# Optimization experiments

Measured on AMD Instinct MI355X. Metric: run time of the kernel, lower is better.

The kernel has to match this reference:

```python
import jax, jax.numpy as jnp
import numpy as np

B, NQ, NP = 4, 8192, 2048
DIM_INP, DIM, HID, OUT, NBLK = 256, 200, 128, 3, 5
VAR = 0.2 ** 2


def setup_inputs() -> dict:
    key = jax.random.key(0)
    ks = jax.random.split(key, 12)
    s = 0.05  # weight scale to keep activations sane
    return {
        "xyz_q": jax.random.uniform(ks[0], (B, NQ, 3), jnp.float32),
        "anchors": jax.random.uniform(ks[1], (B, NP, 3), jnp.float32),
        "anchor_feats": jax.random.normal(ks[2], (B, NP, DIM_INP), jnp.float32),
        "fc0_w": jax.random.normal(ks[3], (DIM_INP, DIM), jnp.float32) * s,
        "fc0_b": jnp.zeros((DIM,), jnp.float32),
        "fc1_w": jax.random.normal(ks[4], (DIM, HID), jnp.float32) * s,
        "fc1_b": jnp.zeros((HID,), jnp.float32),
        "blk_w0": jax.random.normal(ks[5], (NBLK, HID, HID), jnp.float32) * s,
        "blk_b0": jnp.zeros((NBLK, HID), jnp.float32),
        "blk_w1": jax.random.normal(ks[6], (NBLK, HID, HID), jnp.float32) * s,
        "blk_b1": jnp.zeros((NBLK, HID), jnp.float32),
        "fcc_w": jax.random.normal(ks[7], (NBLK, DIM, HID), jnp.float32) * s,
        "fcc_b": jnp.zeros((NBLK, HID), jnp.float32),
        "out_w": jax.random.normal(ks[8], (HID, OUT), jnp.float32) * s,
        "out_b": jnp.zeros((OUT,), jnp.float32),
    }


def reference(xyz_q, anchors, anchor_feats, fc0_w, fc0_b, fc1_w, fc1_b,
              blk_w0, blk_b0, blk_w1, blk_b1, fcc_w, fcc_b, out_w, out_b):
    relu = jax.nn.relu
    # Gaussian-kernel interpolation of anchor features at query points.
    # diff: [B, nq, np, 3]
    diff = anchors[:, None, :, :] - xyz_q[:, :, None, :]
    d = jnp.linalg.norm(diff, axis=-1)                    # [B, nq, np]
    logits = -((d + 1e-5) ** 2) / VAR
    weight = jax.nn.softmax(logits, axis=2)               # exp / sum, stable
    c = jnp.einsum('bqp,bpd->bqd', weight, anchor_feats)  # [B, nq, dim_inp]
    lat = c @ fc0_w + fc0_b                               # [B, nq, dim]
    net = relu(lat) @ fc1_w + fc1_b                       # [B, nq, hid]
    for i in range(NBLK):
        net = net + lat @ fcc_w[i] + fcc_b[i]
        # ResnetBlockFC: x + fc_1(relu(fc_0(relu(x))))
        dx = relu(relu(net) @ blk_w0[i] + blk_b0[i]) @ blk_w1[i] + blk_b1[i]
        net = net + dx
    return relu(net) @ out_w + out_b                      # [B, nq, 3]
```

## Files before the change

### kernel.cpp

```cpp
#include <hip/hip_runtime.h>
#include <math.h>

#define NP     2048
#define NQTOT  8192
#define DIN    256
#define DIM    200
#define HID    128
#define NOUT3  3
#define NBLK   5
#define TQ     32
#define NTHR   256
#define INVVAR 25.0f
#define NKT    (NP / 32)
#define NDT    (DIN / 16)
#define WSCALE 32768.0f
#define NFRAG  760

using f16x8 = __attribute__((ext_vector_type(8))) _Float16;
using f32x4 = __attribute__((ext_vector_type(4))) float;

__device__ __forceinline__ unsigned int pkrtz_u32(float a, float b) {
  auto p = __builtin_amdgcn_cvt_pkrtz(a, b);
  return __builtin_bit_cast(unsigned int, p);
}
__device__ __forceinline__ void pack_f16_2(const float* f, f16x8& h, f16x8& l) {
#pragma unroll
  for (int j = 0; j < 8; ++j) {
    const float v = f[j];
    const _Float16 hh = (_Float16)v;
    h[j] = hh; l[j] = (_Float16)(v - (float)hh);
  }
}
__device__ __forceinline__ void pack_w16(const float* f, f16x8& h, f16x8& l) {
#pragma unroll
  for (int j = 0; j < 8; ++j) {
    const float v = f[j] * WSCALE;
    const _Float16 hh = (_Float16)v;
    h[j] = hh; l[j] = (_Float16)(v - (float)hh);
  }
}
__device__ __forceinline__ void pack_a(const float* f, f16x8& h, f16x8& l) {
  union { f16x8 v; unsigned int u[4]; } H, L;
#pragma unroll
  for (int jp = 0; jp < 4; ++jp) {
    const float a = f[2 * jp], b = f[2 * jp + 1];
    auto hp = __builtin_amdgcn_cvt_pkrtz(a, b);
    H.u[jp] = __builtin_bit_cast(unsigned int, hp);
    L.u[jp] = pkrtz_u32(a - (float)hp[0], b - (float)hp[1]);
  }
  h = H.v; l = L.v;
}
__device__ __forceinline__ unsigned int split_pack(float x) {
  auto hp = __builtin_amdgcn_cvt_pkrtz(x, x);
  return pkrtz_u32(x, x - (float)hp[0]);
}

__device__ __forceinline__ int qsw(int r, int q) {
  return r * TQ + (q ^ (((r >> 2) & 7) << 2));
}
template<int KPAD>
__device__ __forceinline__ int sidx(int q, int k) {
  return q * KPAD + (((k >> 2) ^ (q & 7)) << 2) + (k & 3);
}

template<int KPAD, bool RELU>
__device__ __forceinline__ void store_split4(unsigned int* dst, int k, int qbase, f32x4 v) {
#pragma unroll
  for (int r = 0; r < 4; ++r) {
    float x = v[r];
    if (RELU) x = fmaxf(x, 0.f);
    dst[sidx<KPAD>(qbase + r, k)] = split_pack(x);
  }
}

__global__ __launch_bounds__(NTHR) void pid_packf(const float* __restrict__ F,
                                                  f16x8* __restrict__ wsHi,
                                                  f16x8* __restrict__ wsLo) {
  const int wid = threadIdx.x >> 6, l = threadIdx.x & 63;
  const int tile = blockIdx.x * 4 + wid;
  const int b  = tile >> 10;
  const int kt = (tile >> 4) & 63;
  const int dt = tile & 15;
  const int grp = l >> 4, qn = l & 15;
  const float* src = F + ((size_t)b * NP + kt * 32 + grp * 8) * DIN + dt * 16 + qn;
  float v[8];
#pragma unroll
  for (int j = 0; j < 8; ++j) v[j] = src[(size_t)j * DIN];
  f16x8 h, lo;
  pack_f16_2(v, h, lo);
  const size_t fi = (size_t)tile * 64 + l;
  wsHi[fi] = h; wsLo[fi] = lo;
}

__global__ __launch_bounds__(NTHR) void pid_packw(
    const float* __restrict__ fc0_w, const float* __restrict__ fc1_w,
    const float* __restrict__ fcc_w, const float* __restrict__ blk_w0,
    const float* __restrict__ blk_w1,
    f16x8* __restrict__ Wh, f16x8* __restrict__ Wm) {
  const int wid = threadIdx.x >> 6, l = threadIdx.x & 63;
  const int f = blockIdx.x * 4 + wid;
  if (f >= NFRAG) return;
  const float* src; int Kl, Nl, ks, nt;
  if (f < 104)      { int r = f;       src = fc0_w; Kl = 256; Nl = 200; ks = r / 13; nt = r % 13; }
  else if (f < 160) { int r = f - 104; src = fc1_w; Kl = 200; Nl = 128; ks = r / 8;  nt = r % 8; }
  else if (f < 440) { int r = f - 160; int i = r / 56; r %= 56;
                      src = fcc_w + (size_t)i * DIM * HID; Kl = 200; Nl = 128; ks = r / 8; nt = r % 8; }
  else if (f < 600) { int r = f - 440; int i = r / 32; r %= 32;
                      src = blk_w0 + (size_t)i * HID * HID; Kl = 128; Nl = 128; ks = r / 8; nt = r % 8; }
  else              { int r = f - 600; int i = r / 32; r %= 32;
                      src = blk_w1 + (size_t)i * HID * HID; Kl = 128; Nl = 128; ks = r / 8; nt = r % 8; }
  const int grp = l >> 4, n = nt * 16 + (l & 15);
  f16x8 h, m;
#pragma unroll
  for (int j = 0; j < 8; ++j) {
    const int k = ks * 32 + grp * 8 + j;
    const float v = (k < Kl && n < Nl) ? src[(size_t)k * Nl + n] : 0.f;
    const _Float16 hh = (_Float16)v;
    h[j] = hh; m[j] = (_Float16)(v - (float)hh);
  }
  const size_t fi = (size_t)f * 64 + l;
  Wh[fi] = h; Wm[fi] = m;
}

template<int KS, int NT, int MAXNT, int KPADIN, bool RELUA>
__device__ __forceinline__ void mm_stage(
    const unsigned int* __restrict__ Xs,
    const f16x8* __restrict__ Wh, const f16x8* __restrict__ Wm, int fbase,
    f32x4 acc[2][MAXNT], int wid, int l) {
  const int grp = l >> 4, qn = l & 15;
#pragma unroll 1
  for (int ks = 0; ks < KS; ++ks) {
    f16x8 bh[MAXNT], bm[MAXNT];
#pragma unroll
    for (int i = 0; i < MAXNT; ++i) {
      const int nt = wid + i * 4;
      if (nt < NT) {
        const size_t fi = (size_t)(fbase + ks * NT + nt) * 64 + l;
        bh[i] = Wh[fi]; bm[i] = Wm[fi];
      }
    }
    const int u0 = ks * 8 + grp * 2;
    f16x8 ah[2], al[2];
#pragma unroll
    for (int qt = 0; qt < 2; ++qt) {
      const int q = qt * 16 + qn;
      const unsigned int* row = Xs + q * KPADIN;
      const uint4 lo = *(const uint4*)(row + (((u0) ^ (q & 7)) << 2));
      const uint4 hi = *(const uint4*)(row + (((u0 + 1) ^ (q & 7)) << 2));
      unsigned int p[8] = {lo.x, lo.y, lo.z, lo.w, hi.x, hi.y, hi.z, hi.w};
      if (RELUA) {
#pragma unroll
        for (int j = 0; j < 8; ++j) p[j] = (p[j] & 0x8000u) ? 0u : p[j];
      }
      union { f16x8 v; unsigned int u[4]; } H, L;
#pragma unroll
      for (int jp = 0; jp < 4; ++jp) {
        H.u[jp] = __builtin_amdgcn_perm(p[2 * jp + 1], p[2 * jp], 0x05040100u);
        L.u[jp] = __builtin_amdgcn_perm(p[2 * jp + 1], p[2 * jp], 0x07060302u);
      }
      ah[qt] = H.v; al[qt] = L.v;
    }
#pragma unroll
    for (int qt = 0; qt < 2; ++qt)
#pragma unroll
      for (int i = 0; i < MAXNT; ++i)
        if (wid + i * 4 < NT) {
          acc[qt][i] = __builtin_amdgcn_mfma_f32_16x16x32_f16(ah[qt], bh[i], acc[qt][i], 0, 0, 0);
          acc[qt][i] = __builtin_amdgcn_mfma_f32_16x16x32_f16(ah[qt], bm[i], acc[qt][i], 0, 0, 0);
          acc[qt][i] = __builtin_amdgcn_mfma_f32_16x16x32_f16(al[qt], bh[i], acc[qt][i], 0, 0, 0);
        }
  }
}

struct SMemV2 {
  union {
    struct { float ax[NP * 3]; float qx[TQ], qy[TQ], qz[TQ]; } a;
    unsigned int lats[32 * 224];
  } r1;
  union {
    unsigned int cTs[32 * 256];
    struct { unsigned int nets[32 * 128]; unsigned int tmps[32 * 128]; } nt;
    float netf[128 * 32];
  } r2;
  float sS[64];
};

__global__ __launch_bounds__(NTHR, 2) void pid_fused_mfma(
    const float* __restrict__ xyz_q, const float* __restrict__ anchors,
    const f16x8* __restrict__ wsFh, const f16x8* __restrict__ wsFl,
    const f16x8* __restrict__ Wh, const f16x8* __restrict__ Wm,
    const float* __restrict__ fc0_b, const float* __restrict__ fc1_b,
    const float* __restrict__ blk_b0, const float* __restrict__ blk_b1,
    const float* __restrict__ fcc_b,
    const float* __restrict__ out_w, const float* __restrict__ out_b,
    float* __restrict__ out) {
  __shared__ SMemV2 sm;
  const int t = threadIdx.x;
  const int bi = blockIdx.x;
  const int batch = bi & 3;
  const int q0 = (bi >> 2) * TQ;

  {
    const float4* src = (const float4*)(anchors + (size_t)batch * NP * 3);
    float4* dst = (float4*)sm.r1.a.ax;
#pragma unroll
    for (int j = 0; j < (NP * 3 / 4) / NTHR; ++j)
      dst[j * NTHR + t] = src[j * NTHR + t];
  }
  if (t < TQ) {
    const float* qp = xyz_q + ((size_t)batch * NQTOT + q0 + t) * 3;
    sm.r1.a.qx[t] = qp[0]; sm.r1.a.qy[t] = qp[1]; sm.r1.a.qz[t] = qp[2];
  }
  __syncthreads();

  const int wid = t >> 6, l = t & 63;
  const int kp = wid & 1;
  const int dh = wid >> 1;
  const int grp = l >> 4, qn = l & 15;
  const float q0x = sm.r1.a.qx[qn],      q0y = sm.r1.a.qy[qn],      q0z = sm.r1.a.qz[qn];
  const float q1x = sm.r1.a.qx[16 + qn], q1y = sm.r1.a.qy[16 + qn], q1z = sm.r1.a.qz[16 + qn];
  const float nC1 = -36.067376f;
  const float nC2 = -7.2134752e-4f;

  const size_t fb = (size_t)batch * (NKT * NDT * 64) + kp * 1024 + dh * 512 + l;
  const f16x8* pH0 = wsFh + fb;  const f16x8* pL0 = wsFl + fb;
  const f16x8* pH1 = pH0 + 256;  const f16x8* pL1 = pL0 + 256;

  f32x4 acc[2][8];
#pragma unroll
  for (int a = 0; a < 2; ++a)
#pragma unroll
    for (int j = 0; j < 8; ++j) acc[a][j] = (f32x4){0.f, 0.f, 0.f, 0.f};
  float s0 = 0.f, s1 = 0.f;

#pragma unroll 1
  for (int kt = kp; kt < NKT; kt += 2) {
    const int pb = kt * 32 + grp * 8;
    float4 av[6];
    {
      const float4* ap = (const float4*)&sm.r1.a.ax[pb * 3];
#pragma unroll
      for (int j = 0; j < 6; ++j) av[j] = ap[j];
    }
    const float* af = (const float*)av;
    float w8[8];
#pragma unroll
    for (int j = 0; j < 8; ++j) {
      const float dx = af[3 * j] - q0x, dy = af[3 * j + 1] - q0y, dz = af[3 * j + 2] - q0z;
      const float D = fmaf(dx, dx, fmaf(dy, dy, dz * dz));
      const float s = __builtin_amdgcn_sqrtf(D);
      const float u = __builtin_amdgcn_exp2f(fmaf(nC2, s, fmaf(nC1, D, 15.0f)));
      w8[j] = u; s0 += u;
    }
    f16x8 ah0, al0;
    pack_a(w8, ah0, al0);
#pragma unroll
    for (int j = 0; j < 8; ++j) {
      const float dx = af[3 * j] - q1x, dy = af[3 * j + 1] - q1y, dz = af[3 * j + 2] - q1z;
      const float D = fmaf(dx, dx, fmaf(dy, dy, dz * dz));
      const float s = __builtin_amdgcn_sqrtf(D);
      const float u = __builtin_amdgcn_exp2f(fmaf(nC2, s, fmaf(nC1, D, 15.0f)));
      w8[j] = u; s1 += u;
    }
    f16x8 ah1, al1;
    pack_a(w8, ah1, al1);

#define CHUNK2(PH, PL, DOFF)                                                  \
    {                                                                         \
      f16x8 bh[4], bl[4];                                                     \
      _Pragma("unroll") for (int k = 0; k < 4; ++k) {                         \
        bh[k] = PH[k * 64]; bl[k] = PL[k * 64];                               \
      }                                                                       \
      _Pragma("unroll") for (int k = 0; k < 4; ++k) {                         \
        f32x4 a0 = acc[0][DOFF + k];                                          \
        a0 = __builtin_amdgcn_mfma_f32_16x16x32_f16(ah0, bh[k], a0, 0, 0, 0); \
        a0 = __builtin_amdgcn_mfma_f32_16x16x32_f16(ah0, bl[k], a0, 0, 0, 0); \
        a0 = __builtin_amdgcn_mfma_f32_16x16x32_f16(al0, bh[k], a0, 0, 0, 0); \
        acc[0][DOFF + k] = a0;                                                \
        f32x4 a1 = acc[1][DOFF + k];                                          \
        a1 = __builtin_amdgcn_mfma_f32_16x16x32_f16(ah1, bh[k], a1, 0, 0, 0); \
        a1 = __builtin_amdgcn_mfma_f32_16x16x32_f16(ah1, bl[k], a1, 0, 0, 0); \
        a1 = __builtin_amdgcn_mfma_f32_16x16x32_f16(al1, bh[k], a1, 0, 0, 0); \
        acc[1][DOFF + k] = a1;                                                \
      }                                                                       \
    }
    CHUNK2(pH0, pL0, 0)
    CHUNK2(pH1, pL1, 4)
#undef CHUNK2
    pH0 += 2048; pL0 += 2048; pH1 += 2048; pL1 += 2048;
  }

  s0 += __shfl_xor(s0, 16); s0 += __shfl_xor(s0, 32);
  s1 += __shfl_xor(s1, 16); s1 += __shfl_xor(s1, 32);
  if (dh == 0 && l < 16) {
    sm.sS[kp * 32 + qn] = s0;
    sm.sS[kp * 32 + 16 + qn] = s1;
  }
  float4* P = (float4*)sm.r2.cTs;
  if (kp == 0) {
#pragma unroll
    for (int qt2 = 0; qt2 < 2; ++qt2)
#pragma unroll
      for (int d2 = 0; d2 < 8; ++d2)
        P[(qt2 * 16 + dh * 8 + d2) * 64 + grp * 16 + qn] =
            make_float4(acc[qt2][d2][0], acc[qt2][d2][1],
                        acc[qt2][d2][2], acc[qt2][d2][3]);
  }
  __syncthreads();
  if (kp == 1) {
#pragma unroll
    for (int qt2 = 0; qt2 < 2; ++qt2)
#pragma unroll
      for (int d2 = 0; d2 < 8; ++d2) {
        const float4 pv = P[(qt2 * 16 + dh * 8 + d2) * 64 + grp * 16 + qn];
        acc[qt2][d2][0] += pv.x; acc[qt2][d2][1] += pv.y;
        acc[qt2][d2][2] += pv.z; acc[qt2][d2][3] += pv.w;
      }
  } else {
    const int lid = (wid >> 1) * 64 + l;
#pragma unroll
    for (int z = 0; z < 6; ++z) {
      const int idx = lid * 6 + z;
      const int q = idx / 24, kk = 200 + idx % 24;
      sm.r1.lats[sidx<224>(q, kk)] = 0u;
    }
  }
  __syncthreads();
  if (kp == 1) {
    float sc0[4], sc1[4];
#pragma unroll
    for (int r = 0; r < 4; ++r) {
      const int j = grp * 4 + r;
      sc0[r] = __builtin_amdgcn_rcpf(sm.sS[j] + sm.sS[32 + j]);
      sc1[r] = __builtin_amdgcn_rcpf(sm.sS[16 + j] + sm.sS[48 + j]);
    }
#pragma unroll
    for (int d2 = 0; d2 < 8; ++d2) {
      const int k = (dh * 8 + d2) * 16 + qn;
      const f32x4 v0 = {acc[0][d2][0] * sc0[0], acc[0][d2][1] * sc0[1],
                        acc[0][d2][2] * sc0[2], acc[0][d2][3] * sc0[3]};
      store_split4<256, false>(sm.r2.cTs, k, grp * 4, v0);
      const f32x4 v1 = {acc[1][d2][0] * sc1[0], acc[1][d2][1] * sc1[1],
                        acc[1][d2][2] * sc1[2], acc[1][d2][3] * sc1[3]};
      store_split4<256, false>(sm.r2.cTs, k, 16 + grp * 4, v1);
    }
  }
  __syncthreads();

  {
    f32x4 a0[2][4];
#pragma unroll
    for (int i = 0; i < 4; ++i) {
      const int nt = wid + i * 4;
      if (nt < 13) {
        const int n = nt * 16 + qn;
        const float b = (n < 200) ? fc0_b[n] : 0.f;
#pragma unroll
        for (int q2 = 0; q2 < 2; ++q2) a0[q2][i] = (f32x4){b, b, b, b};
      }
    }
    mm_stage<8, 13, 4, 256, false>(sm.r2.cTs, Wh, Wm, 0, a0, wid, l);
#pragma unroll
    for (int q2 = 0; q2 < 2; ++q2)
#pragma unroll
      for (int i = 0; i < 4; ++i) {
        const int nt = wid + i * 4;
        if (nt < 13)
          store_split4<224, false>(sm.r1.lats, nt * 16 + qn, q2 * 16 + grp * 4, a0[q2][i]);
      }
  }
  __syncthreads();

  f32x4 net[2][2];
#pragma unroll
  for (int i = 0; i < 2; ++i) {
    const float b = fc1_b[(wid + i * 4) * 16 + qn];
#pragma unroll
    for (int q2 = 0; q2 < 2; ++q2) net[q2][i] = (f32x4){b, b, b, b};
  }
  mm_stage<7, 8, 2, 224, true>(sm.r1.lats, Wh, Wm, 104, net, wid, l);

#pragma unroll 1
  for (int ib = 0; ib < NBLK; ++ib) {
#pragma unroll
    for (int i = 0; i < 2; ++i) {
      const float b = fcc_b[ib * HID + (wid + i * 4) * 16 + qn];
#pragma unroll
      for (int q2 = 0; q2 < 2; ++q2) net[q2][i] += (f32x4){b, b, b, b};
    }
    mm_stage<7, 8, 2, 224, false>(sm.r1.lats, Wh, Wm, 160 + 56 * ib, net, wid, l);
#pragma unroll
    for (int q2 = 0; q2 < 2; ++q2)
#pragma unroll
      for (int i = 0; i < 2; ++i)
        store_split4<128, true>(sm.r2.nt.nets, (wid + i * 4) * 16 + qn,
                                q2 * 16 + grp * 4, net[q2][i]);
    __syncthreads();
    f32x4 a2[2][2];
#pragma unroll
    for (int i = 0; i < 2; ++i) {
      const float b = blk_b0[ib * HID + (wid + i * 4) * 16 + qn];
#pragma unroll
      for (int q2 = 0; q2 < 2; ++q2) a2[q2][i] = (f32x4){b, b, b, b};
    }
    mm_stage<4, 8, 2, 128, false>(sm.r2.nt.nets, Wh, Wm, 440 + 32 * ib, a2, wid, l);
#pragma unroll
    for (int q2 = 0; q2 < 2; ++q2)
#pragma unroll
      for (int i = 0; i < 2; ++i)
        store_split4<128, true>(sm.r2.nt.tmps, (wid + i * 4) * 16 + qn,
                                q2 * 16 + grp * 4, a2[q2][i]);
    __syncthreads();
#pragma unroll
    for (int i = 0; i < 2; ++i) {
      const float b = blk_b1[ib * HID + (wid + i * 4) * 16 + qn];
#pragma unroll
      for (int q2 = 0; q2 < 2; ++q2) net[q2][i] += (f32x4){b, b, b, b};
    }
    mm_stage<4, 8, 2, 128, false>(sm.r2.nt.tmps, Wh, Wm, 600 + 32 * ib, net, wid, l);
    __syncthreads();
  }

#pragma unroll
  for (int q2 = 0; q2 < 2; ++q2)
#pragma unroll
    for (int i = 0; i < 2; ++i) {
      const int n = (wid + i * 4) * 16 + qn;
      *(float4*)&sm.r2.netf[n * 32 + q2 * 16 + grp * 4] =
          make_float4(net[q2][i][0], net[q2][i][1], net[q2][i][2], net[q2][i][3]);
    }
  __syncthreads();
  if (t < TQ * NOUT3) {
    const int q = t / NOUT3, n = t - q * NOUT3;
    float s = out_b[n];
#pragma unroll 8
    for (int k = 0; k < HID; ++k)
      s = fmaf(fmaxf(sm.r2.netf[k * 32 + q], 0.f), out_w[k * NOUT3 + n], s);
    out[((size_t)batch * NQTOT + q0 + q) * NOUT3 + n] = s;
  }
}

template<int K, bool RELUX, bool ACCY>
__device__ __forceinline__ void stage_h128(const float* __restrict__ X,
                                           const float* __restrict__ Wg,
                                           const float* __restrict__ bg,
                                           float* __restrict__ Y, int t) {
  const int qg = t & 7, ng = t >> 3;
  const int n0 = ng * 4, q0 = qg * 4;
  const float4 bv = *(const float4*)&bg[n0];
  const float br[4] = {bv.x, bv.y, bv.z, bv.w};
  float acc[4][4];
#pragma unroll
  for (int j = 0; j < 4; ++j) {
    if (ACCY) {
      const float4 yv = *(const float4*)&Y[qsw(n0 + j, q0)];
      acc[0][j] = yv.x + br[j]; acc[1][j] = yv.y + br[j];
      acc[2][j] = yv.z + br[j]; acc[3][j] = yv.w + br[j];
    } else {
      acc[0][j] = br[j]; acc[1][j] = br[j]; acc[2][j] = br[j]; acc[3][j] = br[j];
    }
  }
#pragma unroll 2
  for (int k0 = 0; k0 < K; k0 += 8) {
    float4 wr[8];
#pragma unroll
    for (int kk = 0; kk < 8; ++kk)
      wr[kk] = *(const float4*)&Wg[(size_t)(k0 + kk) * HID + n0];
#pragma unroll
    for (int kk = 0; kk < 8; ++kk) {
      float4 xv = *(const float4*)&X[qsw(k0 + kk, q0)];
      if (RELUX) {
        xv.x = fmaxf(xv.x, 0.f); xv.y = fmaxf(xv.y, 0.f);
        xv.z = fmaxf(xv.z, 0.f); xv.w = fmaxf(xv.w, 0.f);
      }
      const float xr[4] = {xv.x, xv.y, xv.z, xv.w};
      const float wl[4] = {wr[kk].x, wr[kk].y, wr[kk].z, wr[kk].w};
#pragma unroll
      for (int i = 0; i < 4; ++i)
#pragma unroll
        for (int j = 0; j < 4; ++j)
          acc[i][j] = fmaf(xr[i], wl[j], acc[i][j]);
    }
  }
#pragma unroll
  for (int j = 0; j < 4; ++j)
    *(float4*)&Y[qsw(n0 + j, q0)] =
        make_float4(acc[0][j], acc[1][j], acc[2][j], acc[3][j]);
}

__device__ __forceinline__ void stage_fc0v(const float* __restrict__ X,
                                           const float* __restrict__ Wg,
                                           const float* __restrict__ bg,
                                           float* __restrict__ Y, int t) {
  const int qg = t & 7, ng = t >> 3;
  const int n0 = ng * 8, q0 = qg * 4;
  const bool act = (ng < 25);
  float acc[4][8];
  if (act) {
    const float4 b0 = *(const float4*)&bg[n0];
    const float4 b1 = *(const float4*)&bg[n0 + 4];
    const float br[8] = {b0.x, b0.y, b0.z, b0.w, b1.x, b1.y, b1.z, b1.w};
#pragma unroll
    for (int j = 0; j < 8; ++j)
#pragma unroll
      for (int i = 0; i < 4; ++i) acc[i][j] = br[j];
  }
#pragma unroll 2
  for (int k0 = 0; k0 < DIN; k0 += 4) {
    if (act) {
      float4 wa[4], wb[4];
#pragma unroll
      for (int kk = 0; kk < 4; ++kk) {
        wa[kk] = *(const float4*)&Wg[(size_t)(k0 + kk) * DIM + n0];
        wb[kk] = *(const float4*)&Wg[(size_t)(k0 + kk) * DIM + n0 + 4];
      }
#pragma unroll
      for (int kk = 0; kk < 4; ++kk) {
        const float4 xv = *(const float4*)&X[qsw(k0 + kk, q0)];
        const float xr[4] = {xv.x, xv.y, xv.z, xv.w};
        const float wl[8] = {wa[kk].x, wa[kk].y, wa[kk].z, wa[kk].w,
                             wb[kk].x, wb[kk].y, wb[kk].z, wb[kk].w};
#pragma unroll
        for (int i = 0; i < 4; ++i)
#pragma unroll
          for (int j = 0; j < 8; ++j)
            acc[i][j] = fmaf(xr[i], wl[j], acc[i][j]);
      }
    }
  }
  if (act) {
#pragma unroll
    for (int j = 0; j < 8; ++j)
      *(float4*)&Y[qsw(n0 + j, q0)] =
          make_float4(acc[0][j], acc[1][j], acc[2][j], acc[3][j]);
  }
}

struct SA1 {
  float ax[NP * 3];
  float qx[TQ], qy[TQ], qz[TQ], m[TQ];
  float sred[8 * TQ];
};
struct SB1 {
  float lat[DIM * TQ];
  union {
    float cT[DIN * TQ];
    struct { float net[HID * TQ]; float tmp[HID * TQ]; } nt;
  } u;
};
struct SMem1 { union { SA1 a; SB1 b; } s; float sS[TQ]; };

__global__ __launch_bounds__(NTHR, 2) void pid_fused_vec(
    const float* __restrict__ xyz_q, const float* __restrict__ anchors,
    const f16x8* __restrict__ wsFh, const f16x8* __restrict__ wsFl,
    const float* __restrict__ fc0_w, const float* __restrict__ fc0_b,
    const float* __restrict__ fc1_w, const float* __restrict__ fc1_b,
    const float* __restrict__ blk_w0, const float* __restrict__ blk_b0,
    const float* __restrict__ blk_w1, const float* __restrict__ blk_b1,
    const float* __restrict__ fcc_w, const float* __restrict__ fcc_b,
    const float* __restrict__ out_w, const float* __restrict__ out_b,
    float* __restrict__ out) {
  __shared__ SMem1 sm;
  const int t = threadIdx.x;
  const int bi = blockIdx.x;
  const int batch = bi & 3;
  const int q0 = (bi >> 2) * TQ;

  {
    const float4* src = (const float4*)(anchors + (size_t)batch * NP * 3);
    float4* dst = (float4*)sm.s.a.ax;
#pragma unroll
    for (int j = 0; j < (NP * 3 / 4) / NTHR; ++j)
      dst[j * NTHR + t] = src[j * NTHR + t];
  }
  if (t < TQ) {
    const float* qp = xyz_q + ((size_t)batch * NQTOT + q0 + t) * 3;
    sm.s.a.qx[t] = qp[0]; sm.s.a.qy[t] = qp[1]; sm.s.a.qz[t] = qp[2];
  }
  __syncthreads();
  {
    const int q = t & 31, g = t >> 5;
    const float qxv = sm.s.a.qx[q], qyv = sm.s.a.qy[q], qzv = sm.s.a.qz[q];
    float mloc = 3.0e38f;
    const float* az = sm.s.a.ax + g * 256 * 3;
    for (int pi = 0; pi < 256; ++pi) {
      const float dx = az[pi * 3 + 0] - qxv;
      const float dy = az[pi * 3 + 1] - qyv;
      const float dz = az[pi * 3 + 2] - qzv;
      mloc = fminf(mloc, fmaf(dx, dx, fmaf(dy, dy, dz * dz)));
    }
    sm.s.a.sred[g * TQ + q] = mloc;
  }
  __syncthreads();
  if (t < TQ) {
    float mv = sm.s.a.sred[t];
#pragma unroll
    for (int g = 1; g < 8; ++g) mv = fminf(mv, sm.s.a.sred[g * TQ + t]);
    const float dmin = sqrtf(mv) + 1e-5f;
    sm.s.a.m[t] = -dmin * dmin * INVVAR;
  }
  __syncthreads();

  const int wid = t >> 6, l = t & 63;
  const int qt = wid & 1;
  const int dgb = (wid >> 1) * 8;
  const int grp = l >> 4, qn = l & 15;
  const float qxv = sm.s.a.qx[qt * 16 + qn];
  const float qyv = sm.s.a.qy[qt * 16 + qn];
  const float qzv = sm.s.a.qz[qt * 16 + qn];
  const float negm = -sm.s.a.m[qt * 16 + qn];
  const f16x8* BH = wsFh + (size_t)batch * NKT * NDT * 64;
  const f16x8* BL = wsFl + (size_t)batch * NKT * NDT * 64;

  f32x4 acc[8];
#pragma unroll
  for (int j = 0; j < 8; ++j) acc[j] = (f32x4){0.f, 0.f, 0.f, 0.f};
  float ssum = 0.f;
#pragma unroll 1
  for (int kt = 0; kt < NKT; ++kt) {
    f16x8 bh[8], bl[8];
#pragma unroll
    for (int d2 = 0; d2 < 8; ++d2) {
      const size_t fi = ((size_t)kt * NDT + dgb + d2) * 64 + l;
      bh[d2] = BH[fi]; bl[d2] = BL[fi];
    }
    const int pb = kt * 32 + grp * 8;
    float4 av[6];
    {
      const float4* ap = (const float4*)&sm.s.a.ax[pb * 3];
#pragma unroll
      for (int j = 0; j < 6; ++j) av[j] = ap[j];
    }
    const float* af = (const float*)av;
    float w8[8];
#pragma unroll
    for (int j = 0; j < 8; ++j) {
      const float dx = af[3 * j] - qxv, dy = af[3 * j + 1] - qyv, dz = af[3 * j + 2] - qzv;
      const float d = sqrtf(fmaf(dx, dx, fmaf(dy, dy, dz * dz))) + 1e-5f;
      const float u = __expf(fmaf(d * d, -INVVAR, negm));
      w8[j] = u; ssum += u;
    }
    f16x8 ah, al;
    pack_w16(w8, ah, al);
#pragma unroll
    for (int d2 = 0; d2 < 8; ++d2)
      acc[d2] = __builtin_amdgcn_mfma_f32_16x16x32_f16(ah, bh[d2], acc[d2], 0, 0, 0);
#pragma unroll
    for (int d2 = 0; d2 < 8; ++d2)
      acc[d2] = __builtin_amdgcn_mfma_f32_16x16x32_f16(ah, bl[d2], acc[d2], 0, 0, 0);
#pragma unroll
    for (int d2 = 0; d2 < 8; ++d2)
      acc[d2] = __builtin_amdgcn_mfma_f32_16x16x32_f16(al, bh[d2], acc[d2], 0, 0, 0);
  }
  ssum += __shfl_xor(ssum, 16);
  ssum += __shfl_xor(ssum, 32);
  if (wid < 2 && grp == 0) sm.sS[qt * 16 + qn] = ssum;
  __syncthreads();
  float sc[4];
#pragma unroll
  for (int r = 0; r < 4; ++r)
    sc[r] = (1.0f / WSCALE) / sm.sS[qt * 16 + grp * 4 + r];
#pragma unroll
  for (int d2 = 0; d2 < 8; ++d2) {
    const int d = (dgb + d2) * 16 + qn;
    *(float4*)&sm.s.b.u.cT[qsw(d, qt * 16 + grp * 4)] =
        make_float4(acc[d2][0] * sc[0], acc[d2][1] * sc[1],
                    acc[d2][2] * sc[2], acc[d2][3] * sc[3]);
  }
  __syncthreads();

  stage_fc0v(sm.s.b.u.cT, fc0_w, fc0_b, sm.s.b.lat, t);
  __syncthreads();
  stage_h128<DIM, true, false>(sm.s.b.lat, fc1_w, fc1_b, sm.s.b.u.nt.net, t);
  __syncthreads();
#pragma unroll 1
  for (int i = 0; i < NBLK; ++i) {
    stage_h128<DIM, false, true>(sm.s.b.lat, fcc_w + (size_t)i * DIM * HID,
                                 fcc_b + i * HID, sm.s.b.u.nt.net, t);
    __syncthreads();
    stage_h128<HID, true, false>(sm.s.b.u.nt.net, blk_w0 + (size_t)i * HID * HID,
                                 blk_b0 + i * HID, sm.s.b.u.nt.tmp, t);
    __syncthreads();
    stage_h128<HID, true, true>(sm.s.b.u.nt.tmp, blk_w1 + (size_t)i * HID * HID,
                                blk_b1 + i * HID, sm.s.b.u.nt.net, t);
    __syncthreads();
  }
  if (t < TQ * NOUT3) {
    const int q = t / NOUT3, n = t - q * NOUT3;
    float s = out_b[n];
    const float* net = sm.s.b.u.nt.net;
#pragma unroll 8
    for (int k = 0; k < HID; ++k)
      s = fmaf(fmaxf(net[k * TQ + (q ^ (((k >> 2) & 7) << 2))], 0.f),
               out_w[k * NOUT3 + n], s);
    out[((size_t)batch * NQTOT + q0 + q) * NOUT3 + n] = s;
  }
}

extern "C" void kernel_launch(void* const* d_in, const int* in_sizes, int n_in,
                              void* d_out, int out_size, void* d_ws, size_t ws_size,
                              hipStream_t stream) {
  (void)in_sizes; (void)n_in; (void)out_size;
  const float* xyz_q        = (const float*)d_in[0];
  const float* anchors      = (const float*)d_in[1];
  const float* anchor_feats = (const float*)d_in[2];
  const float* fc0_w        = (const float*)d_in[3];
  const float* fc0_b        = (const float*)d_in[4];
  const float* fc1_w        = (const float*)d_in[5];
  const float* fc1_b        = (const float*)d_in[6];
  const float* blk_w0       = (const float*)d_in[7];
  const float* blk_b0       = (const float*)d_in[8];
  const float* blk_w1       = (const float*)d_in[9];
  const float* blk_b1       = (const float*)d_in[10];
  const float* fcc_w        = (const float*)d_in[11];
  const float* fcc_b        = (const float*)d_in[12];
  const float* out_w        = (const float*)d_in[13];
  const float* out_b        = (const float*)d_in[14];
  float* out = (float*)d_out;

  const size_t F_BYTES = (size_t)4 * NKT * NDT * 64 * 16;
  const size_t W_BYTES = (size_t)NFRAG * 64 * 16;
  f16x8* wsFh = (f16x8*)d_ws;
  f16x8* wsFl = (f16x8*)((char*)d_ws + F_BYTES);
  f16x8* Wh   = (f16x8*)((char*)d_ws + 2 * F_BYTES);
  f16x8* Wm   = (f16x8*)((char*)d_ws + 2 * F_BYTES + W_BYTES);

  hipLaunchKernelGGL(pid_packf, dim3(1024), dim3(NTHR), 0, stream,
                     anchor_feats, wsFh, wsFl);
  if (ws_size >= 2 * F_BYTES + 2 * W_BYTES) {
    hipLaunchKernelGGL(pid_packw, dim3((NFRAG + 3) / 4), dim3(NTHR), 0, stream,
                       fc0_w, fc1_w, fcc_w, blk_w0, blk_w1, Wh, Wm);
    hipLaunchKernelGGL(pid_fused_mfma, dim3(1024), dim3(NTHR), 0, stream,
                       xyz_q, anchors, wsFh, wsFl, Wh, Wm,
                       fc0_b, fc1_b, blk_b0, blk_b1, fcc_b, out_w, out_b, out);
  } else {
    hipLaunchKernelGGL(pid_fused_vec, dim3(1024), dim3(NTHR), 0, stream,
                       xyz_q, anchors, wsFh, wsFl,
                       fc0_w, fc0_b, fc1_w, fc1_b, blk_w0, blk_b0,
                       blk_w1, blk_b1, fcc_w, fcc_b, out_w, out_b, out);
  }
}
```

Before: 262.4 us.

## Prefetch MFMA weight fragments ahead of compute and drop per-block barrier

The MLP stage helper now double-buffers its weight fragments, loading the next k-step's fragments from global memory while MFMAs run on the current ones. The interpolation loop issues all eight weight-fragment loads at the top of each iteration, before the distance and exp work, so global latency hides behind ALU work. The trailing __syncthreads inside the residual-block loop moves after the loop. Each change targets exposed memory latency or barrier stalls, at the cost of more live VGPRs (spill or occupancy risk under launch_bounds 2) and a possible shared-memory race between consecutive blocks if that barrier was needed.

```diff
diff --git a/kernel.cpp b/kernel.cpp
--- a/kernel.cpp
+++ b/kernel.cpp
@@ -128,48 +128,58 @@
     const f16x8* __restrict__ Wh, const f16x8* __restrict__ Wm, int fbase,
     f32x4 acc[2][MAXNT], int wid, int l) {
   const int grp = l >> 4, qn = l & 15;
+  f16x8 bhA[MAXNT], bmA[MAXNT], bhB[MAXNT], bmB[MAXNT];
+
+#define LOADF(BH, BM, KSV)                                                    \
+  _Pragma("unroll") for (int i = 0; i < MAXNT; ++i) {                         \
+    const int nt = wid + i * 4;                                               \
+    if (nt < NT) {                                                            \
+      const size_t fi = (size_t)(fbase + (KSV) * NT + nt) * 64 + l;           \
+      BH[i] = Wh[fi]; BM[i] = Wm[fi];                                         \
+    }                                                                         \
+  }
+
+#define COMPUTE(KSV, BH, BM)                                                  \
+  {                                                                           \
+    const int u0 = (KSV) * 8 + grp * 2;                                       \
+    f16x8 ah[2], al[2];                                                       \
+    _Pragma("unroll") for (int qt = 0; qt < 2; ++qt) {                        \
+      const int q = qt * 16 + qn;                                             \
+      const unsigned int* row = Xs + q * KPADIN;                              \
+      const uint4 lo = *(const uint4*)(row + (((u0) ^ (q & 7)) << 2));        \
+      const uint4 hi = *(const uint4*)(row + (((u0 + 1) ^ (q & 7)) << 2));    \
+      unsigned int p[8] = {lo.x, lo.y, lo.z, lo.w, hi.x, hi.y, hi.z, hi.w};   \
+      if (RELUA) {                                                            \
+        _Pragma("unroll") for (int j = 0; j < 8; ++j)                         \
+          p[j] = (p[j] & 0x8000u) ? 0u : p[j];                                \
+      }                                                                       \
+      union { f16x8 v; unsigned int u[4]; } H, L;                             \
+      _Pragma("unroll") for (int jp = 0; jp < 4; ++jp) {                      \
+        H.u[jp] = __builtin_amdgcn_perm(p[2 * jp + 1], p[2 * jp], 0x05040100u);\
+        L.u[jp] = __builtin_amdgcn_perm(p[2 * jp + 1], p[2 * jp], 0x07060302u);\
+      }                                                                       \
+      ah[qt] = H.v; al[qt] = L.v;                                             \
+    }                                                                         \
+    _Pragma("unroll") for (int qt = 0; qt < 2; ++qt)                          \
+    _Pragma("unroll") for (int i = 0; i < MAXNT; ++i)                         \
+      if (wid + i * 4 < NT) {                                                 \
+        acc[qt][i] = __builtin_amdgcn_mfma_f32_16x16x32_f16(ah[qt], BH[i], acc[qt][i], 0, 0, 0); \
+        acc[qt][i] = __builtin_amdgcn_mfma_f32_16x16x32_f16(ah[qt], BM[i], acc[qt][i], 0, 0, 0); \
+        acc[qt][i] = __builtin_amdgcn_mfma_f32_16x16x32_f16(al[qt], BH[i], acc[qt][i], 0, 0, 0); \
+      }                                                                       \
+  }
+
+  LOADF(bhA, bmA, 0)
 #pragma unroll 1
-  for (int ks = 0; ks < KS; ++ks) {
-    f16x8 bh[MAXNT], bm[MAXNT];
-#pragma unroll
-    for (int i = 0; i < MAXNT; ++i) {
-      const int nt = wid + i * 4;
-      if (nt < NT) {
-        const size_t fi = (size_t)(fbase + ks * NT + nt) * 64 + l;
-        bh[i] = Wh[fi]; bm[i] = Wm[fi];
-      }
-    }
-    const int u0 = ks * 8 + grp * 2;
-    f16x8 ah[2], al[2];
-#pragma unroll
-    for (int qt = 0; qt < 2; ++qt) {
-      const int q = qt * 16 + qn;
-      const unsigned int* row = Xs + q * KPADIN;
-      const uint4 lo = *(const uint4*)(row + (((u0) ^ (q & 7)) << 2));
-      const uint4 hi = *(const uint4*)(row + (((u0 + 1) ^ (q & 7)) << 2));
-      unsigned int p[8] = {lo.x, lo.y, lo.z, lo.w, hi.x, hi.y, hi.z, hi.w};
-      if (RELUA) {
-#pragma unroll
-        for (int j = 0; j < 8; ++j) p[j] = (p[j] & 0x8000u) ? 0u : p[j];
-      }
-      union { f16x8 v; unsigned int u[4]; } H, L;
-#pragma unroll
-      for (int jp = 0; jp < 4; ++jp) {
-        H.u[jp] = __builtin_amdgcn_perm(p[2 * jp + 1], p[2 * jp], 0x05040100u);
-        L.u[jp] = __builtin_amdgcn_perm(p[2 * jp + 1], p[2 * jp], 0x07060302u);
-      }
-      ah[qt] = H.v; al[qt] = L.v;
-    }
-#pragma unroll
-    for (int qt = 0; qt < 2; ++qt)
-#pragma unroll
-      for (int i = 0; i < MAXNT; ++i)
-        if (wid + i * 4 < NT) {
-          acc[qt][i] = __builtin_amdgcn_mfma_f32_16x16x32_f16(ah[qt], bh[i], acc[qt][i], 0, 0, 0);
-          acc[qt][i] = __builtin_amdgcn_mfma_f32_16x16x32_f16(ah[qt], bm[i], acc[qt][i], 0, 0, 0);
-          acc[qt][i] = __builtin_amdgcn_mfma_f32_16x16x32_f16(al[qt], bh[i], acc[qt][i], 0, 0, 0);
-        }
-  }
+  for (int ks = 0; ks + 1 < KS; ks += 2) {
+    LOADF(bhB, bmB, ks + 1)
+    COMPUTE(ks, bhA, bmA)
+    if (ks + 2 < KS) { LOADF(bhA, bmA, ks + 2) }
+    COMPUTE(ks + 1, bhB, bmB)
+  }
+  if (KS & 1) { COMPUTE(KS - 1, bhA, bmA) }
+#undef LOADF
+#undef COMPUTE
 }
 
 struct SMemV2 {
@@ -235,6 +245,12 @@
 
 #pragma unroll 1
   for (int kt = kp; kt < NKT; kt += 2) {
+    f16x8 bh0[4], bl0[4], bh1[4], bl1[4];
+#pragma unroll
+    for (int k = 0; k < 4; ++k) { bh0[k] = pH0[k * 64]; bl0[k] = pL0[k * 64]; }
+#pragma unroll
+    for (int k = 0; k < 4; ++k) { bh1[k] = pH1[k * 64]; bl1[k] = pL1[k * 64]; }
+
     const int pb = kt * 32 + grp * 8;
     float4 av[6];
     {
@@ -265,28 +281,21 @@
     f16x8 ah1, al1;
     pack_a(w8, ah1, al1);
 
-#define CHUNK2(PH, PL, DOFF)                                                  \
-    {                                                                         \
-      f16x8 bh[4], bl[4];                                                     \
-      _Pragma("unroll") for (int k = 0; k < 4; ++k) {                         \
-        bh[k] = PH[k * 64]; bl[k] = PL[k * 64];                               \
-      }                                                                       \
-      _Pragma("unroll") for (int k = 0; k < 4; ++k) {                         \
-        f32x4 a0 = acc[0][DOFF + k];                                          \
-        a0 = __builtin_amdgcn_mfma_f32_16x16x32_f16(ah0, bh[k], a0, 0, 0, 0); \
-        a0 = __builtin_amdgcn_mfma_f32_16x16x32_f16(ah0, bl[k], a0, 0, 0, 0); \
-        a0 = __builtin_amdgcn_mfma_f32_16x16x32_f16(al0, bh[k], a0, 0, 0, 0); \
-        acc[0][DOFF + k] = a0;                                                \
-        f32x4 a1 = acc[1][DOFF + k];                                          \
-        a1 = __builtin_amdgcn_mfma_f32_16x16x32_f16(ah1, bh[k], a1, 0, 0, 0); \
-        a1 = __builtin_amdgcn_mfma_f32_16x16x32_f16(ah1, bl[k], a1, 0, 0, 0); \
-        a1 = __builtin_amdgcn_mfma_f32_16x16x32_f16(al1, bh[k], a1, 0, 0, 0); \
-        acc[1][DOFF + k] = a1;                                                \
-      }                                                                       \
-    }
-    CHUNK2(pH0, pL0, 0)
-    CHUNK2(pH1, pL1, 4)
-#undef CHUNK2
+#define MM3(ACC, AH, AL, BH, BL)                                              \
+    ACC = __builtin_amdgcn_mfma_f32_16x16x32_f16(AH, BH, ACC, 0, 0, 0);       \
+    ACC = __builtin_amdgcn_mfma_f32_16x16x32_f16(AH, BL, ACC, 0, 0, 0);       \
+    ACC = __builtin_amdgcn_mfma_f32_16x16x32_f16(AL, BH, ACC, 0, 0, 0);
+#pragma unroll
+    for (int k = 0; k < 4; ++k) {
+      MM3(acc[0][k], ah0, al0, bh0[k], bl0[k])
+      MM3(acc[1][k], ah1, al1, bh0[k], bl0[k])
+    }
+#pragma unroll
+    for (int k = 0; k < 4; ++k) {
+      MM3(acc[0][4 + k], ah0, al0, bh1[k], bl1[k])
+      MM3(acc[1][4 + k], ah1, al1, bh1[k], bl1[k])
+    }
+#undef MM3
     pH0 += 2048; pL0 += 2048; pH1 += 2048; pL1 += 2048;
   }
 
@@ -418,8 +427,8 @@
       for (int q2 = 0; q2 < 2; ++q2) net[q2][i] += (f32x4){b, b, b, b};
     }
     mm_stage<4, 8, 2, 128, false>(sm.r2.nt.tmps, Wh, Wm, 600 + 32 * ib, net, wid, l);
-    __syncthreads();
-  }
+  }
+  __syncthreads();
 
 #pragma unroll
   for (int q2 = 0; q2 < 2; ++q2)
```

New measurement: 252.6 us. 3.7% less time.
